# Optimization experiments

Hardware: AMD Instinct MI355X
Metric: run time of the kernel (lower is better)

The kernel has to match this reference:

```python
import jax, jax.numpy as jnp
import numpy as np

B, R = 2, 4096
N_COARSE, N_IMP = 48, 48
RAY_START, RAY_END = 0.1, 1.0
BOX_WARP = 2.0
C_PLANE, H_PLANE = 32, 256
HIDDEN = 64

_P = np.array([[[1, 0, 0], [0, 1, 0], [0, 0, 1]],
               [[1, 0, 0], [0, 0, 1], [0, 1, 0]],
               [[0, 0, 1], [1, 0, 0], [0, 1, 0]]], np.float32)
INV_PLANES = jnp.asarray(np.linalg.inv(_P))  # [3,3,3]


def _gs_one(f, g):
    # f: [C,H,W]; g: [M,2] in [-1,1]; bilinear, zeros padding, align_corners=False
    C, H, W = f.shape
    x = (g[:, 0] + 1.0) * (W / 2) - 0.5
    y = (g[:, 1] + 1.0) * (H / 2) - 0.5
    x0 = jnp.floor(x); y0 = jnp.floor(y)
    xi0 = x0.astype(jnp.int32); yi0 = y0.astype(jnp.int32)
    fx = x - x0; fy = y - y0
    out = jnp.zeros((C, g.shape[0]), f.dtype)
    for dx in (0, 1):
        for dy in (0, 1):
            xi = xi0 + dx; yi = yi0 + dy
            w = (fx if dx else 1.0 - fx) * (fy if dy else 1.0 - fy)
            valid = (xi >= 0) & (xi < W) & (yi >= 0) & (yi < H)
            val = f[:, jnp.clip(yi, 0, H - 1), jnp.clip(xi, 0, W - 1)]  # [C,M]
            out = out + jnp.where(valid, w, 0.0)[None, :] * val
    return out

grid_sample_2d = jax.vmap(_gs_one)


def sample_from_planes(plane_feats, coords):
    # plane_feats [B,3,C,H,W], coords [B,M,3] -> [B,M,C] (mean over planes)
    b, nP, C, H, W = plane_feats.shape
    c = (2.0 / BOX_WARP) * coords
    proj = jnp.einsum('bmk,pkj->bpmj', c, INV_PLANES)[..., :2]  # [B,3,M,2]
    out = grid_sample_2d(plane_feats.reshape(b * nP, C, H, W), proj.reshape(b * nP, -1, 2))
    return out.reshape(b, nP, C, -1).mean(1).transpose(0, 2, 1)


def decoder(tex_f, shp_f, W1, b1, W2, b2):
    x = jnp.concatenate([tex_f, shp_f], -1)          # [B,M,2C]
    h = jax.nn.softplus(x @ W1 + b1)
    o = h @ W2 + b2
    sigma = o[..., :1]
    rgb = jax.nn.sigmoid(o[..., 1:]) * (1 + 2 * 0.001) - 0.001
    return rgb, sigma


def ray_march(colors, densities, depths):
    # MipRayMarcher2: midpoint compositing, softplus(density-1), alpha compositing
    deltas = depths[:, :, 1:] - depths[:, :, :-1]
    c_mid = (colors[:, :, :-1] + colors[:, :, 1:]) * 0.5
    d_mid = (densities[:, :, :-1] + densities[:, :, 1:]) * 0.5
    z_mid = (depths[:, :, :-1] + depths[:, :, 1:]) * 0.5
    dens = jax.nn.softplus(d_mid - 1.0)
    alpha = 1.0 - jnp.exp(-dens * deltas)
    shifted = jnp.concatenate([jnp.ones_like(alpha[:, :, :1]), 1.0 - alpha + 1e-10], 2)
    weights = alpha * jnp.cumprod(shifted, 2)[:, :, :-1]
    rgb = (weights * c_mid).sum(2)
    wt = weights.sum(2)
    depth = jnp.nan_to_num((weights * z_mid).sum(2) / wt, posinf=0.0)
    depth = jnp.clip(depth, depths.min(), depths.max())
    return rgb * 2.0 - 1.0, depth, weights


def sample_pdf(bins, weights, u):
    # bins [P,Nb], weights [P,Nw], u [P,Ni] -> inverse-CDF samples [P,Ni]
    pdf = weights / jnp.sum(weights, -1, keepdims=True)
    cdf = jnp.cumsum(pdf, -1)
    cdf = jnp.concatenate([jnp.zeros_like(cdf[:, :1]), cdf], -1)
    inds = jax.vmap(lambda c, uu: jnp.searchsorted(c, uu, side='right'))(cdf, u)
    below = jnp.maximum(inds - 1, 0)
    above = jnp.minimum(inds, weights.shape[-1])
    cdf0 = jnp.take_along_axis(cdf, below, 1)
    cdf1 = jnp.take_along_axis(cdf, above, 1)
    b0 = jnp.take_along_axis(bins, below, 1)
    b1v = jnp.take_along_axis(bins, above, 1)
    denom = cdf1 - cdf0
    denom = jnp.where(denom < 1e-5, 1.0, denom)
    t = (u - cdf0) / denom
    return b0 + t * (b1v - b0)


def sample_importance(depths, weights, u):
    b, r, n1, _ = weights.shape  # n1 = N_COARSE - 1
    w = weights.reshape(b * r, n1)
    # max_pool1d(k=2, s=1, pad=1) then avg_pool1d(k=2, s=1), then +0.01 (weights >= 0)
    wp = jnp.concatenate([jnp.zeros_like(w[:, :1]), w, jnp.zeros_like(w[:, :1])], 1)
    w = jnp.maximum(wp[:, :-1], wp[:, 1:])
    w = 0.5 * (w[:, :-1] + w[:, 1:]) + 0.01
    z = depths.reshape(b * r, -1)
    z_mid = 0.5 * (z[:, :-1] + z[:, 1:])
    fine = sample_pdf(z_mid, w[:, 1:-1], u.reshape(b * r, -1))
    return jax.lax.stop_gradient(fine.reshape(b, r, -1, 1))  # .detach() in torch


def run_model(planes_tex, planes_shp, coords, W1, b1, W2, b2):
    tex_f = sample_from_planes(planes_tex, coords)
    shp_f = sample_from_planes(planes_shp, coords)
    return decoder(tex_f, shp_f, W1, b1, W2, b2)


def reference(planes_tex, planes_shp, ray_origins, ray_directions, W1, b1, W2, b2, strat_noise, imp_u):
    dirs = ray_directions / jnp.linalg.norm(ray_directions, axis=-1, keepdims=True)
    b, r, _ = ray_origins.shape
    delta = (RAY_END - RAY_START) / (N_COARSE - 1)
    base = RAY_START + delta * jnp.arange(N_COARSE, dtype=jnp.float32)
    depths_c = base.reshape(1, 1, N_COARSE, 1) + strat_noise * delta  # [B,R,Nc,1]
    coords_c = (ray_origins[:, :, None] + depths_c * dirs[:, :, None]).reshape(b, -1, 3)
    rgb_c, sig_c = run_model(planes_tex, planes_shp, coords_c, W1, b1, W2, b2)
    rgb_c = rgb_c.reshape(b, r, N_COARSE, 3)
    sig_c = sig_c.reshape(b, r, N_COARSE, 1)
    _, _, weights = ray_march(rgb_c, sig_c, depths_c)
    depths_f = sample_importance(depths_c, weights, imp_u)  # [B,R,Ni,1]
    coords_f = (ray_origins[:, :, None] + depths_f * dirs[:, :, None]).reshape(b, -1, 3)
    rgb_f, sig_f = run_model(planes_tex, planes_shp, coords_f, W1, b1, W2, b2)
    rgb_f = rgb_f.reshape(b, r, N_IMP, 3)
    sig_f = sig_f.reshape(b, r, N_IMP, 1)
    all_d = jnp.concatenate([depths_c, depths_f], 2)
    all_c = jnp.concatenate([rgb_c, rgb_f], 2)
    all_s = jnp.concatenate([sig_c, sig_f], 2)
    idx = jnp.argsort(all_d, axis=2)
    all_d = jnp.take_along_axis(all_d, idx, 2)
    all_c = jnp.take_along_axis(all_c, jnp.broadcast_to(idx, all_c.shape), 2)
    all_s = jnp.take_along_axis(all_s, idx, 2)
    rgb_final, depth_final, w_all = ray_march(all_c, all_s, all_d)
    return rgb_final, depth_final, w_all.sum(2)


def setup_inputs() -> dict:
    key = jax.random.key(0)
    ks = jax.random.split(key, 8)
    return {
        'planes_tex': jax.random.normal(ks[0], (B, 3, C_PLANE, H_PLANE, H_PLANE), jnp.float32),
        'planes_shp': jax.random.normal(ks[1], (B, 3, C_PLANE, H_PLANE, H_PLANE), jnp.float32),
        'ray_origins': 0.3 * jax.random.normal(ks[2], (B, R, 3), jnp.float32),
        'ray_directions': jax.random.normal(ks[3], (B, R, 3), jnp.float32),
        'W1': jax.random.normal(ks[4], (2 * C_PLANE, HIDDEN), jnp.float32) / np.sqrt(2 * C_PLANE),
        'b1': jnp.zeros((HIDDEN,), jnp.float32),
        'W2': jax.random.normal(ks[5], (HIDDEN, 4), jnp.float32) / np.sqrt(HIDDEN),
        'b2': jnp.zeros((4,), jnp.float32),
        'strat_noise': jax.random.uniform(ks[6], (B, R, N_COARSE, 1), jnp.float32),
        'imp_u': jax.random.uniform(ks[7], (B, R, N_IMP), jnp.float32),
    }
```

## Files before the change

kernel.cpp:

```cpp
#include <hip/hip_runtime.h>
#include <hip/hip_fp16.h>
#include <math.h>

#define NRAY 8192
#define NC_  48
#define NI_  48
#define CPL  32
#define HPL  256
#define HID  64
#define NPTS (NRAY * NC_)

typedef __attribute__((ext_vector_type(8))) short short8;
typedef __attribute__((ext_vector_type(4))) float f32x4;

__device__ __forceinline__ float softplusf(float x) {
    return fmaxf(x, 0.0f) + __logf(1.0f + __expf(-fabsf(x)));
}
__device__ __forceinline__ float sigmoidf(float x) {
    return 1.0f / (1.0f + __expf(-x));
}
__device__ __forceinline__ unsigned short f2bf(float f) {
    unsigned u = __float_as_uint(f);
    u += 0x7fffu + ((u >> 16) & 1u);
    return (unsigned short)(u >> 16);
}

#define TR_BLOCKS 3072
__global__ __launch_bounds__(256) void setup_kernel(
    const float* __restrict__ tex, const float* __restrict__ shp,
    __half* __restrict__ planes_cl,
    const float* __restrict__ W1, const float* __restrict__ b1, const float* __restrict__ W2,
    unsigned short* __restrict__ w1f, float* __restrict__ w2f, float* __restrict__ b1f,
    float* __restrict__ minmax,
    const float* __restrict__ noise, float* __restrict__ depths)
{
    __shared__ __half t2[256][34];
    int b = blockIdx.x;
    int tid = threadIdx.x;
    if (b < TR_BLOCKS) {
        int p = b >> 8;
        int y = b & 255;
        const float* in = (p < 6) ? tex : shp;
        int pp    = (p < 6) ? p : p - 6;
        int choff = (p < 6) ? 0 : 32;
        const float* row = in + ((size_t)(pp * 32) * 256 + y) * 256;
#pragma unroll
        for (int c = 0; c < 32; ++c)
            t2[tid][c] = __float2half(row[(size_t)c * 65536 + tid]);
        __syncthreads();
        __half* outRow = planes_cl + ((size_t)(pp * 256 + y) * 256) * 64 + choff;
#pragma unroll
        for (int it = 0; it < 4; ++it) {
            int idx = it * 256 + tid;
            int x = idx >> 2, c8 = (idx & 3) * 8;
            *(uint4*)(outRow + (size_t)x * 64 + c8) = *(const uint4*)&t2[x][c8];
        }
    } else if (b == TR_BLOCKS) {
        int l = tid;
        if (l == 0) {
            ((int*)minmax)[0] = 0x7f800000;
            ((int*)minmax)[1] = 0xff800000;
        }
        if (l < 64) {
            int g = l >> 4, c = l & 15;
#pragma unroll
            for (int t = 0; t < 4; ++t) {
#pragma unroll
                for (int kb = 0; kb < 2; ++kb)
#pragma unroll
                    for (int j = 0; j < 8; ++j)
                        w1f[((t * 2 + kb) * 64 + l) * 8 + j] =
                            f2bf(W1[(kb * 32 + g * 8 + j) * HID + t * 16 + c]);
#pragma unroll
                for (int o = 0; o < 4; ++o) w2f[(t * 64 + l) * 4 + o] = W2[(t * 16 + c) * 4 + o];
                b1f[t * 64 + l] = b1[t * 16 + c];
            }
        }
    } else {
        int gid = (b - TR_BLOCKS - 1) * 256 + tid;
        if (gid < NPTS) {
            int s = gid % NC_;
            const float delta = (1.0f - 0.1f) / (NC_ - 1);
            depths[gid] = 0.1f + delta * (float)s + noise[gid] * delta;
        }
    }
}

__global__ __launch_bounds__(256, 8) void fused_sample_mlp(
    const __half* __restrict__ planes,
    const float* __restrict__ origins, const float* __restrict__ dirs,
    const float* __restrict__ depths,
    const unsigned short* __restrict__ w1f, const float* __restrict__ w2f,
    const float* __restrict__ b1f, const float* __restrict__ b2,
    float4* __restrict__ outRGBS)
{
    __shared__ unsigned short lds_x[32][72];
    __shared__ int s_tap[32][12][2];

    int tid = threadIdx.x;

    if (tid < 96) {
        int p  = tid & 31;
        int pp = tid >> 5;
        int point = blockIdx.x * 32 + p;
        int ray = point / NC_;
        int bIdx = ray >> 12;

        float ox = origins[ray * 3 + 0], oy = origins[ray * 3 + 1], oz = origins[ray * 3 + 2];
        float dx = dirs[ray * 3 + 0], dy = dirs[ray * 3 + 1], dz = dirs[ray * 3 + 2];
        float invn = 1.0f / sqrtf(dx * dx + dy * dy + dz * dz);
        dx *= invn; dy *= invn; dz *= invn;
        float t = depths[point];
        float px = ox + t * dx, py = oy + t * dy, pz = oz + t * dz;

        float U = (pp == 2) ? pz : px;
        float V = (pp == 0) ? py : ((pp == 1) ? pz : px);
        const float inv3 = 1.0f / 3.0f;

        float gx = (U + 1.0f) * 128.0f - 0.5f;
        float gy = (V + 1.0f) * 128.0f - 0.5f;
        float fgx = floorf(gx), fgy = floorf(gy);
        int x0 = (int)fgx, y0 = (int)fgy;
        float fx = gx - fgx, fy = gy - fgy;
#pragma unroll
        for (int k = 0; k < 4; ++k) {
            int dxk = k & 1, dyk = k >> 1;
            int xi = x0 + dxk, yi = y0 + dyk;
            float w = (dxk ? fx : 1.0f - fx) * (dyk ? fy : 1.0f - fy);
            bool valid = (xi >= 0) && (xi < HPL) && (yi >= 0) && (yi < HPL);
            int xc = min(max(xi, 0), HPL - 1);
            int yc = min(max(yi, 0), HPL - 1);
            int p3 = bIdx * 3 + pp;
            s_tap[p][pp * 4 + k][0] = (((p3 * HPL) + yc) * HPL + xc) * 64;
            s_tap[p][pp * 4 + k][1] = __float_as_int(valid ? w * inv3 : 0.0f);
        }
    }
    __syncthreads();

    {
        int p = tid >> 3, sub = tid & 7;
        int   off[12];
        float wv[12];
#pragma unroll
        for (int kk = 0; kk < 12; ++kk) {
            off[kk] = s_tap[p][kk][0];
            wv[kk]  = __int_as_float(s_tap[p][kk][1]);
        }
        __half2 acc2[4];
#pragma unroll
        for (int i = 0; i < 4; ++i) acc2[i] = __half2half2(__float2half(0.0f));
#pragma unroll
        for (int kk = 0; kk < 12; ++kk) {
            __half2 w2 = __half2half2(__float2half(wv[kk]));
            float4 v = *(const float4*)(planes + off[kk] + sub * 8);
            union { float4 f; __half2 h[4]; } u;
            u.f = v;
#pragma unroll
            for (int i = 0; i < 4; ++i) acc2[i] = __hfma2(u.h[i], w2, acc2[i]);
        }
        unsigned short u16[8];
#pragma unroll
        for (int i = 0; i < 4; ++i) {
            float2 f2 = __half22float2(acc2[i]);
            u16[2 * i]     = f2bf(f2.x);
            u16[2 * i + 1] = f2bf(f2.y);
        }
        *(uint4*)&lds_x[p][sub * 8] = *(uint4*)(u16);
    }
    __syncthreads();

    int lane = tid & 63, wave = tid >> 6;
    if (wave < 2) {
        int g = lane >> 4, c = lane & 15;
        int mrow = wave * 16 + c;
        short8 a0 = *(const short8*)(&lds_x[mrow][g * 8]);
        short8 a1 = *(const short8*)(&lds_x[mrow][32 + g * 8]);

        float o[4][4];
#pragma unroll
        for (int r = 0; r < 4; ++r)
#pragma unroll
            for (int q = 0; q < 4; ++q) o[r][q] = 0.0f;

#pragma unroll
        for (int t = 0; t < 4; ++t) {
            short8 bf0 = *(const short8*)(w1f + ((size_t)((t * 2 + 0) * 64 + lane)) * 8);
            short8 bf1 = *(const short8*)(w1f + ((size_t)((t * 2 + 1) * 64 + lane)) * 8);
            f32x4 z = {0.f, 0.f, 0.f, 0.f};
            z = __builtin_amdgcn_mfma_f32_16x16x32_bf16(a0, bf0, z, 0, 0, 0);
            z = __builtin_amdgcn_mfma_f32_16x16x32_bf16(a1, bf1, z, 0, 0, 0);
            float  b1s = b1f[t * 64 + lane];
            float4 w2  = *(const float4*)(w2f + (size_t)(t * 64 + lane) * 4);
#pragma unroll
            for (int r = 0; r < 4; ++r) {
                float sp = softplusf(z[r] + b1s);
                o[r][0] = fmaf(sp, w2.x, o[r][0]);
                o[r][1] = fmaf(sp, w2.y, o[r][1]);
                o[r][2] = fmaf(sp, w2.z, o[r][2]);
                o[r][3] = fmaf(sp, w2.w, o[r][3]);
            }
        }
#pragma unroll
        for (int mask = 1; mask <= 8; mask <<= 1)
#pragma unroll
            for (int r = 0; r < 4; ++r)
#pragma unroll
                for (int q = 0; q < 4; ++q) o[r][q] += __shfl_xor(o[r][q], mask, 64);

        if (c == 0) {
#pragma unroll
            for (int r = 0; r < 4; ++r) {
                int pt = blockIdx.x * 32 + wave * 16 + g * 4 + r;
                float sig = o[r][0] + b2[0];
                float rr = sigmoidf(o[r][1] + b2[1]) * 1.002f - 0.001f;
                float gg = sigmoidf(o[r][2] + b2[2]) * 1.002f - 0.001f;
                float bb = sigmoidf(o[r][3] + b2[3]) * 1.002f - 0.001f;
                outRGBS[pt] = make_float4(rr, gg, bb, sig);
            }
        }
    }
}

#define CI_WAVES 4
__global__ __launch_bounds__(256) void cdf_imp(
    const float* __restrict__ depths_c, const float4* __restrict__ rgbs_c,
    const float* __restrict__ impu,
    float* __restrict__ depths_f, float* __restrict__ minmax)
{
    __shared__ float s_cdf[CI_WAVES][48];
    __shared__ float s_zm[CI_WAVES][48];
    __shared__ float smn[CI_WAVES], smx[CI_WAVES];
    int wave = threadIdx.x >> 6, lane = threadIdx.x & 63;
    int ray = blockIdx.x * CI_WAVES + wave;

    float d = 0.f, sg = 0.f;
    if (lane < NC_) {
        d  = depths_c[ray * NC_ + lane];
        sg = rgbs_c[ray * NC_ + lane].w;
    }
    float dn = __shfl_down(d, 1, 64);
    float sn = __shfl_down(sg, 1, 64);
    bool iv = (lane < NC_ - 1);

    float zm = 0.5f * (d + dn);
    float alpha = 0.f, f = 1.0f;
    if (iv) {
        float dens = softplusf(0.5f * (sg + sn) - 1.0f);
        alpha = 1.0f - __expf(-dens * (dn - d));
        f = 1.0f - alpha + 1e-10f;
    }
    float x = f;
#pragma unroll
    for (int s = 1; s < 64; s <<= 1) {
        float t = __shfl_up(x, s, 64);
        if (lane >= s) x *= t;
    }
    float excl = __shfl_up(x, 1, 64);
    if (lane == 0) excl = 1.0f;
    float w = alpha * excl;

    float wprev = __shfl_up(w, 1, 64);
    float wmax;
    if (lane == 0) wmax = w;
    else if (lane == NC_ - 1) wmax = wprev;
    else wmax = fmaxf(wprev, w);
    float wmaxn = __shfl_down(wmax, 1, 64);
    float wb = 0.5f * (wmax + wmaxn) + 0.01f;

    float v = (lane >= 1 && lane <= 45) ? wb : 0.0f;
    float s = v;
#pragma unroll
    for (int mask = 1; mask <= 32; mask <<= 1) s += __shfl_xor(s, mask, 64);
    float pdf = v / s;
    float cum = pdf;
#pragma unroll
    for (int st = 1; st < 64; st <<= 1) {
        float t = __shfl_up(cum, st, 64);
        if (lane >= st) cum += t;
    }
    if (lane <= 45) s_cdf[wave][lane] = (lane == 0) ? 0.0f : cum;
    if (iv) s_zm[wave][lane] = zm;

    float d47 = __shfl(d, NC_ - 1, 64);
    if (lane == 0) { smn[wave] = d; smx[wave] = d47; }
    __syncthreads();
    if (threadIdx.x == 0) {
        float mn = smn[0], mx = smx[0];
#pragma unroll
        for (int i = 1; i < CI_WAVES; ++i) { mn = fminf(mn, smn[i]); mx = fmaxf(mx, smx[i]); }
        atomicMin((int*)minmax, __float_as_int(mn));
        atomicMax(((int*)minmax) + 1, __float_as_int(mx));
    }

    if (lane < NI_) {
        const float* cdf = s_cdf[wave];
        const float* zmp = s_zm[wave];
        float u = impu[ray * NI_ + lane];
        int lo = 0, hi = 46;
        while (lo < hi) { int mid = (lo + hi) >> 1; if (cdf[mid] > u) hi = mid; else lo = mid + 1; }
        int below = max(lo - 1, 0);
        int above = min(lo, 45);
        float c0 = cdf[below], c1 = cdf[above];
        float b0 = zmp[below], b1v = zmp[above];
        float den = c1 - c0; if (den < 1e-5f) den = 1.0f;
        depths_f[ray * NI_ + lane] = b0 + (u - c0) / den * (b1v - b0);
    }
}

#define FM_WAVES 4
__global__ __launch_bounds__(256) void final_march(
    const float* __restrict__ depths_c, const float4* __restrict__ rgbs_c,
    const float* __restrict__ depths_f, const float4* __restrict__ rgbs_f,
    const float* __restrict__ minmax, float* __restrict__ out)
{
    __shared__ float s_dc[FM_WAVES][NC_];
    __shared__ float s_df[FM_WAVES][NI_];
    __shared__ float s_md[FM_WAVES][96];
    __shared__ float s_ms[FM_WAVES][96];
    __shared__ float s_mr[FM_WAVES][96];
    __shared__ float s_mg[FM_WAVES][96];
    __shared__ float s_mb[FM_WAVES][96];

    int wave = threadIdx.x >> 6, lane = threadIdx.x & 63;
    int ray = blockIdx.x * FM_WAVES + wave;
    float* dcp = s_dc[wave];
    float* dfp = s_df[wave];
    float* mdp = s_md[wave];
    float* msp = s_ms[wave];
    float* mrp = s_mr[wave];
    float* mgp = s_mg[wave];
    float* mbp = s_mb[wave];

    float dcv = 0.f, dfv = 0.f;
    float4 c4 = make_float4(0, 0, 0, 0), f4 = make_float4(0, 0, 0, 0);
    if (lane < NC_) {
        dcv = depths_c[ray * NC_ + lane];
        dfv = depths_f[ray * NI_ + lane];
        dcp[lane] = dcv;
        dfp[lane] = dfv;
        c4 = rgbs_c[ray * NC_ + lane];
        f4 = rgbs_f[ray * NI_ + lane];
    }
    __syncthreads();

    if (lane < NC_) {
        int cntC = 0, rankF = 0, cntCle = 0;
#pragma unroll
        for (int j = 0; j < NC_; ++j) {
            float dfj = dfp[j];
            float dcj = dcp[j];
            cntC   += (dfj < dcv) ? 1 : 0;
            rankF  += ((dfj < dfv) || (dfj == dfv && j < lane)) ? 1 : 0;
            cntCle += (dcj <= dfv) ? 1 : 0;
        }
        int posC = lane + cntC;
        int posF = rankF + cntCle;
        mdp[posC] = dcv; msp[posC] = c4.w; mrp[posC] = c4.x; mgp[posC] = c4.y; mbp[posC] = c4.z;
        mdp[posF] = dfv; msp[posF] = f4.w; mrp[posF] = f4.x; mgp[posF] = f4.y; mbp[posF] = f4.z;
    }
    __syncthreads();

    int k0 = 2 * lane;
    int i0 = min(k0, 95), i1 = min(k0 + 1, 95), i2 = min(k0 + 2, 95);
    float d0 = mdp[i0], d1 = mdp[i1], d2 = mdp[i2];
    float sg0 = msp[i0], sg1 = msp[i1], sg2 = msp[i2];
    float r0 = mrp[i0], r1 = mrp[i1], r2 = mrp[i2];
    float g0 = mgp[i0], g1 = mgp[i1], g2 = mgp[i2];
    float bb0 = mbp[i0], bb1 = mbp[i1], bb2 = mbp[i2];

    bool v0 = (k0 < 95), v1 = (k0 + 1 < 95);
    float a0 = 0.f, a1 = 0.f, f0 = 1.f, f1 = 1.f;
    if (v0) {
        float dens = softplusf(0.5f * (sg0 + sg1) - 1.0f);
        a0 = 1.0f - __expf(-dens * (d1 - d0));
        f0 = 1.0f - a0 + 1e-10f;
    }
    if (v1) {
        float dens = softplusf(0.5f * (sg1 + sg2) - 1.0f);
        a1 = 1.0f - __expf(-dens * (d2 - d1));
        f1 = 1.0f - a1 + 1e-10f;
    }

    float pl = f0 * f1;
    float x = pl;
#pragma unroll
    for (int d = 1; d < 64; d <<= 1) {
        float t = __shfl_up(x, d, 64);
        if (lane >= d) x *= t;
    }
    float excl = __shfl_up(x, 1, 64);
    if (lane == 0) excl = 1.0f;
    float w0 = a0 * excl;
    float w1 = a1 * excl * f0;

    float accR = w0 * 0.5f * (r0 + r1) + w1 * 0.5f * (r1 + r2);
    float accG = w0 * 0.5f * (g0 + g1) + w1 * 0.5f * (g1 + g2);
    float accB = w0 * 0.5f * (bb0 + bb1) + w1 * 0.5f * (bb1 + bb2);
    float accD = w0 * 0.5f * (d0 + d1) + w1 * 0.5f * (d1 + d2);
    float accW = w0 + w1;
#pragma unroll
    for (int mask = 1; mask <= 32; mask <<= 1) {
        accR += __shfl_xor(accR, mask, 64);
        accG += __shfl_xor(accG, mask, 64);
        accB += __shfl_xor(accB, mask, 64);
        accD += __shfl_xor(accD, mask, 64);
        accW += __shfl_xor(accW, mask, 64);
    }

    if (lane == 0) {
        float q = accD / accW;
        if (!isfinite(q)) q = 0.0f;
        q = fminf(fmaxf(q, minmax[0]), minmax[1]);
        out[ray * 3 + 0] = accR * 2.0f - 1.0f;
        out[ray * 3 + 1] = accG * 2.0f - 1.0f;
        out[ray * 3 + 2] = accB * 2.0f - 1.0f;
        out[3 * NRAY + ray] = q;
        out[4 * NRAY + ray] = accW;
    }
}

extern "C" void kernel_launch(void* const* d_in, const int* in_sizes, int n_in,
                              void* d_out, int out_size, void* d_ws, size_t ws_size,
                              hipStream_t stream)
{
    const float* planes_tex = (const float*)d_in[0];
    const float* planes_shp = (const float*)d_in[1];
    const float* origins    = (const float*)d_in[2];
    const float* raydirs    = (const float*)d_in[3];
    const float* W1 = (const float*)d_in[4];
    const float* b1 = (const float*)d_in[5];
    const float* W2 = (const float*)d_in[6];
    const float* b2 = (const float*)d_in[7];
    const float* noise = (const float*)d_in[8];
    const float* impu  = (const float*)d_in[9];
    float* out = (float*)d_out;

    char* ws = (char*)d_ws;
    __half*         planes_cl = (__half*)ws;
    unsigned short* w1f       = (unsigned short*)(ws + 50331648);
    float*          w2f       = (float*)(ws + 50339840);
    float*          b1f       = (float*)(ws + 50343936);
    float*          minmax    = (float*)(ws + 50345216);
    float*  depths_c = (float*)(ws + 50345472);
    float*  depths_f = depths_c + NPTS;
    float4* rgbs_c   = (float4*)(depths_f + NPTS);
    float4* rgbs_f   = rgbs_c + NPTS;

    int fill_blocks = (NPTS + 255) / 256;
    setup_kernel<<<dim3(TR_BLOCKS + 1 + fill_blocks), dim3(256), 0, stream>>>(
        planes_tex, planes_shp, planes_cl, W1, b1, W2, w1f, w2f, b1f, minmax, noise, depths_c);

    fused_sample_mlp<<<dim3(NPTS / 32), dim3(256), 0, stream>>>(
        planes_cl, origins, raydirs, depths_c, w1f, w2f, b1f, b2, rgbs_c);

    cdf_imp<<<dim3(NRAY / CI_WAVES), dim3(256), 0, stream>>>(depths_c, rgbs_c, impu, depths_f, minmax);

    fused_sample_mlp<<<dim3(NPTS / 32), dim3(256), 0, stream>>>(
        planes_cl, origins, raydirs, depths_f, w1f, w2f, b1f, b2, rgbs_f);

    final_march<<<dim3(NRAY / FM_WAVES), dim3(256), 0, stream>>>(depths_c, rgbs_c, depths_f, rgbs_f, minmax, out);
}
```

Before: 321.2 us.

## Fuse depth generation and importance sampling into the sample-MLP kernels

Coarse depths are now computed inline in the first sample-MLP pass, and the CDF/importance sampling step is folded into the second pass, which builds per-ray CDFs in shared memory before sampling. This removes the separate cdf_imp launch and the depth-fill pass in setup. The global depth min/max atomics are replaced by 16 partial min/max values computed from noise in setup and reduced in final_march. The cost is that each fine block recomputes the CDF for up to two rays, so the same CDF work is redone across blocks, and the block now needs an extra barrier.

```diff
diff --git a/kernel.cpp b/kernel.cpp
--- a/kernel.cpp
+++ b/kernel.cpp
@@ -5,7 +5,6 @@
 #define NRAY 8192
 #define NC_  48
 #define NI_  48
-#define CPL  32
 #define HPL  256
 #define HID  64
 #define NPTS (NRAY * NC_)
@@ -31,10 +30,11 @@
     __half* __restrict__ planes_cl,
     const float* __restrict__ W1, const float* __restrict__ b1, const float* __restrict__ W2,
     unsigned short* __restrict__ w1f, float* __restrict__ w2f, float* __restrict__ b1f,
-    float* __restrict__ minmax,
-    const float* __restrict__ noise, float* __restrict__ depths)
+    float* __restrict__ part_mn, float* __restrict__ part_mx,
+    const float* __restrict__ noise)
 {
     __shared__ __half t2[256][34];
+    __shared__ float smn[4], smx[4];
     int b = blockIdx.x;
     int tid = threadIdx.x;
     if (b < TR_BLOCKS) {
@@ -57,10 +57,6 @@
         }
     } else if (b == TR_BLOCKS) {
         int l = tid;
-        if (l == 0) {
-            ((int*)minmax)[0] = 0x7f800000;
-            ((int*)minmax)[1] = 0xff800000;
-        }
         if (l < 64) {
             int g = l >> 4, c = l & 15;
 #pragma unroll
@@ -77,27 +73,104 @@
             }
         }
     } else {
-        int gid = (b - TR_BLOCKS - 1) * 256 + tid;
-        if (gid < NPTS) {
-            int s = gid % NC_;
+        int bl = b - TR_BLOCKS - 1;
+        int gtid = bl * 256 + tid;
+        float mn = INFINITY, mx = -INFINITY;
+        for (int r = gtid; r < NRAY; r += 4096) {
+            mn = fminf(mn, noise[r * NC_]);
+            mx = fmaxf(mx, noise[r * NC_ + NC_ - 1]);
+        }
+#pragma unroll
+        for (int mask = 1; mask <= 32; mask <<= 1) {
+            mn = fminf(mn, __shfl_xor(mn, mask, 64));
+            mx = fmaxf(mx, __shfl_xor(mx, mask, 64));
+        }
+        int wv = tid >> 6;
+        if ((tid & 63) == 0) { smn[wv] = mn; smx[wv] = mx; }
+        __syncthreads();
+        if (tid == 0) {
+#pragma unroll
+            for (int i = 1; i < 4; ++i) { mn = fminf(mn, smn[i]); mx = fmaxf(mx, smx[i]); }
             const float delta = (1.0f - 0.1f) / (NC_ - 1);
-            depths[gid] = 0.1f + delta * (float)s + noise[gid] * delta;
-        }
-    }
-}
-
+            part_mn[bl] = 0.1f + mn * delta;
+            part_mx[bl] = 0.1f + delta * 47.0f + mx * delta;
+        }
+    }
+}
+
+template<bool FINE>
 __global__ __launch_bounds__(256, 8) void fused_sample_mlp(
     const __half* __restrict__ planes,
     const float* __restrict__ origins, const float* __restrict__ dirs,
-    const float* __restrict__ depths,
+    const float* __restrict__ noise,
+    const float* __restrict__ impu,
+    const float* __restrict__ depths_c,
+    const float4* __restrict__ rgbs_c_in,
+    float* __restrict__ depths_out,
     const unsigned short* __restrict__ w1f, const float* __restrict__ w2f,
     const float* __restrict__ b1f, const float* __restrict__ b2,
     float4* __restrict__ outRGBS)
 {
     __shared__ unsigned short lds_x[32][72];
     __shared__ int s_tap[32][12][2];
+    __shared__ float s_cdf[2][48];
+    __shared__ float s_zm[2][48];
 
     int tid = threadIdx.x;
+    int r0 = (blockIdx.x * 32) / NC_;
+
+    if constexpr (FINE) {
+        int wv = tid >> 6, lane = tid & 63;
+        int r1 = (blockIdx.x * 32 + 31) / NC_;
+        if (wv <= r1 - r0) {
+            int ray = r0 + wv;
+            float d = 0.f, sg = 0.f;
+            if (lane < NC_) {
+                d  = depths_c[ray * NC_ + lane];
+                sg = rgbs_c_in[ray * NC_ + lane].w;
+            }
+            float dn = __shfl_down(d, 1, 64);
+            float sn = __shfl_down(sg, 1, 64);
+            bool iv = (lane < NC_ - 1);
+            float zm = 0.5f * (d + dn);
+            float alpha = 0.f, f = 1.0f;
+            if (iv) {
+                float dens = softplusf(0.5f * (sg + sn) - 1.0f);
+                alpha = 1.0f - __expf(-dens * (dn - d));
+                f = 1.0f - alpha + 1e-10f;
+            }
+            float x = f;
+#pragma unroll
+            for (int s = 1; s < 64; s <<= 1) {
+                float t = __shfl_up(x, s, 64);
+                if (lane >= s) x *= t;
+            }
+            float excl = __shfl_up(x, 1, 64);
+            if (lane == 0) excl = 1.0f;
+            float w = alpha * excl;
+            float wprev = __shfl_up(w, 1, 64);
+            float wmax;
+            if (lane == 0) wmax = w;
+            else if (lane == NC_ - 1) wmax = wprev;
+            else wmax = fmaxf(wprev, w);
+            float wmaxn = __shfl_down(wmax, 1, 64);
+            float wb = 0.5f * (wmax + wmaxn) + 0.01f;
+            float v = (lane >= 1 && lane <= 45) ? wb : 0.0f;
+            float ssum = v;
+#pragma unroll
+            for (int mask = 1; mask <= 32; mask <<= 1) ssum += __shfl_xor(ssum, mask, 64);
+            float pdf = v / ssum;
+            float cum = pdf;
+#pragma unroll
+            for (int st = 1; st < 64; st <<= 1) {
+                float t = __shfl_up(cum, st, 64);
+                if (lane >= st) cum += t;
+            }
+            if (lane <= 45) s_cdf[wv][lane] = (lane == 0) ? 0.0f : cum;
+            if (iv) s_zm[wv][lane] = zm;
+        }
+        __syncthreads();
+    }
 
     if (tid < 96) {
         int p  = tid & 31;
@@ -106,11 +179,31 @@
         int ray = point / NC_;
         int bIdx = ray >> 12;
 
+        float t;
+        if constexpr (!FINE) {
+            int s = point - ray * NC_;
+            const float delta = (1.0f - 0.1f) / (NC_ - 1);
+            t = 0.1f + delta * (float)s + noise[point] * delta;
+        } else {
+            int ridx = ray - r0;
+            float u = impu[point];
+            const float* cdf = s_cdf[ridx];
+            const float* zmp = s_zm[ridx];
+            int lo = 0, hi = 46;
+            while (lo < hi) { int mid = (lo + hi) >> 1; if (cdf[mid] > u) hi = mid; else lo = mid + 1; }
+            int below = max(lo - 1, 0);
+            int above = min(lo, 45);
+            float c0 = cdf[below], c1 = cdf[above];
+            float b0 = zmp[below], b1v = zmp[above];
+            float den = c1 - c0; if (den < 1e-5f) den = 1.0f;
+            t = b0 + (u - c0) / den * (b1v - b0);
+        }
+        if (pp == 0) depths_out[point] = t;
+
         float ox = origins[ray * 3 + 0], oy = origins[ray * 3 + 1], oz = origins[ray * 3 + 2];
         float dx = dirs[ray * 3 + 0], dy = dirs[ray * 3 + 1], dz = dirs[ray * 3 + 2];
         float invn = 1.0f / sqrtf(dx * dx + dy * dy + dz * dz);
         dx *= invn; dy *= invn; dz *= invn;
-        float t = depths[point];
         float px = ox + t * dx, py = oy + t * dy, pz = oz + t * dz;
 
         float U = (pp == 2) ? pz : px;
@@ -221,97 +314,12 @@
     }
 }
 
-#define CI_WAVES 4
-__global__ __launch_bounds__(256) void cdf_imp(
-    const float* __restrict__ depths_c, const float4* __restrict__ rgbs_c,
-    const float* __restrict__ impu,
-    float* __restrict__ depths_f, float* __restrict__ minmax)
-{
-    __shared__ float s_cdf[CI_WAVES][48];
-    __shared__ float s_zm[CI_WAVES][48];
-    __shared__ float smn[CI_WAVES], smx[CI_WAVES];
-    int wave = threadIdx.x >> 6, lane = threadIdx.x & 63;
-    int ray = blockIdx.x * CI_WAVES + wave;
-
-    float d = 0.f, sg = 0.f;
-    if (lane < NC_) {
-        d  = depths_c[ray * NC_ + lane];
-        sg = rgbs_c[ray * NC_ + lane].w;
-    }
-    float dn = __shfl_down(d, 1, 64);
-    float sn = __shfl_down(sg, 1, 64);
-    bool iv = (lane < NC_ - 1);
-
-    float zm = 0.5f * (d + dn);
-    float alpha = 0.f, f = 1.0f;
-    if (iv) {
-        float dens = softplusf(0.5f * (sg + sn) - 1.0f);
-        alpha = 1.0f - __expf(-dens * (dn - d));
-        f = 1.0f - alpha + 1e-10f;
-    }
-    float x = f;
-#pragma unroll
-    for (int s = 1; s < 64; s <<= 1) {
-        float t = __shfl_up(x, s, 64);
-        if (lane >= s) x *= t;
-    }
-    float excl = __shfl_up(x, 1, 64);
-    if (lane == 0) excl = 1.0f;
-    float w = alpha * excl;
-
-    float wprev = __shfl_up(w, 1, 64);
-    float wmax;
-    if (lane == 0) wmax = w;
-    else if (lane == NC_ - 1) wmax = wprev;
-    else wmax = fmaxf(wprev, w);
-    float wmaxn = __shfl_down(wmax, 1, 64);
-    float wb = 0.5f * (wmax + wmaxn) + 0.01f;
-
-    float v = (lane >= 1 && lane <= 45) ? wb : 0.0f;
-    float s = v;
-#pragma unroll
-    for (int mask = 1; mask <= 32; mask <<= 1) s += __shfl_xor(s, mask, 64);
-    float pdf = v / s;
-    float cum = pdf;
-#pragma unroll
-    for (int st = 1; st < 64; st <<= 1) {
-        float t = __shfl_up(cum, st, 64);
-        if (lane >= st) cum += t;
-    }
-    if (lane <= 45) s_cdf[wave][lane] = (lane == 0) ? 0.0f : cum;
-    if (iv) s_zm[wave][lane] = zm;
-
-    float d47 = __shfl(d, NC_ - 1, 64);
-    if (lane == 0) { smn[wave] = d; smx[wave] = d47; }
-    __syncthreads();
-    if (threadIdx.x == 0) {
-        float mn = smn[0], mx = smx[0];
-#pragma unroll
-        for (int i = 1; i < CI_WAVES; ++i) { mn = fminf(mn, smn[i]); mx = fmaxf(mx, smx[i]); }
-        atomicMin((int*)minmax, __float_as_int(mn));
-        atomicMax(((int*)minmax) + 1, __float_as_int(mx));
-    }
-
-    if (lane < NI_) {
-        const float* cdf = s_cdf[wave];
-        const float* zmp = s_zm[wave];
-        float u = impu[ray * NI_ + lane];
-        int lo = 0, hi = 46;
-        while (lo < hi) { int mid = (lo + hi) >> 1; if (cdf[mid] > u) hi = mid; else lo = mid + 1; }
-        int below = max(lo - 1, 0);
-        int above = min(lo, 45);
-        float c0 = cdf[below], c1 = cdf[above];
-        float b0 = zmp[below], b1v = zmp[above];
-        float den = c1 - c0; if (den < 1e-5f) den = 1.0f;
-        depths_f[ray * NI_ + lane] = b0 + (u - c0) / den * (b1v - b0);
-    }
-}
-
 #define FM_WAVES 4
 __global__ __launch_bounds__(256) void final_march(
     const float* __restrict__ depths_c, const float4* __restrict__ rgbs_c,
     const float* __restrict__ depths_f, const float4* __restrict__ rgbs_f,
-    const float* __restrict__ minmax, float* __restrict__ out)
+    const float* __restrict__ part_mn, const float* __restrict__ part_mx,
+    float* __restrict__ out)
 {
     __shared__ float s_dc[FM_WAVES][NC_];
     __shared__ float s_df[FM_WAVES][NI_];
@@ -407,10 +415,18 @@
         accW += __shfl_xor(accW, mask, 64);
     }
 
+    float pmn = (lane < 16) ? part_mn[lane] : INFINITY;
+    float pmx = (lane < 16) ? part_mx[lane] : -INFINITY;
+#pragma unroll
+    for (int mask = 1; mask <= 32; mask <<= 1) {
+        pmn = fminf(pmn, __shfl_xor(pmn, mask, 64));
+        pmx = fmaxf(pmx, __shfl_xor(pmx, mask, 64));
+    }
+
     if (lane == 0) {
         float q = accD / accW;
         if (!isfinite(q)) q = 0.0f;
-        q = fminf(fmaxf(q, minmax[0]), minmax[1]);
+        q = fminf(fmaxf(q, pmn), pmx);
         out[ray * 3 + 0] = accR * 2.0f - 1.0f;
         out[ray * 3 + 1] = accG * 2.0f - 1.0f;
         out[ray * 3 + 2] = accB * 2.0f - 1.0f;
@@ -440,23 +456,24 @@
     unsigned short* w1f       = (unsigned short*)(ws + 50331648);
     float*          w2f       = (float*)(ws + 50339840);
     float*          b1f       = (float*)(ws + 50343936);
-    float*          minmax    = (float*)(ws + 50345216);
-    float*  depths_c = (float*)(ws + 50345472);
-    float*  depths_f = depths_c + NPTS;
-    float4* rgbs_c   = (float4*)(depths_f + NPTS);
-    float4* rgbs_f   = rgbs_c + NPTS;
-
-    int fill_blocks = (NPTS + 255) / 256;
-    setup_kernel<<<dim3(TR_BLOCKS + 1 + fill_blocks), dim3(256), 0, stream>>>(
-        planes_tex, planes_shp, planes_cl, W1, b1, W2, w1f, w2f, b1f, minmax, noise, depths_c);
-
-    fused_sample_mlp<<<dim3(NPTS / 32), dim3(256), 0, stream>>>(
-        planes_cl, origins, raydirs, depths_c, w1f, w2f, b1f, b2, rgbs_c);
-
-    cdf_imp<<<dim3(NRAY / CI_WAVES), dim3(256), 0, stream>>>(depths_c, rgbs_c, impu, depths_f, minmax);
-
-    fused_sample_mlp<<<dim3(NPTS / 32), dim3(256), 0, stream>>>(
-        planes_cl, origins, raydirs, depths_f, w1f, w2f, b1f, b2, rgbs_f);
-
-    final_march<<<dim3(NRAY / FM_WAVES), dim3(256), 0, stream>>>(depths_c, rgbs_c, depths_f, rgbs_f, minmax, out);
-}
+    float*          part_mn   = (float*)(ws + 50344960);
+    float*          part_mx   = (float*)(ws + 50345024);
+    float*  depths_c = (float*)(ws + 50345216);
+    float*  depths_f = (float*)(ws + 51918080);
+    float4* rgbs_c   = (float4*)(ws + 53490944);
+    float4* rgbs_f   = (float4*)(ws + 59782400);
+
+    setup_kernel<<<dim3(TR_BLOCKS + 1 + 16), dim3(256), 0, stream>>>(
+        planes_tex, planes_shp, planes_cl, W1, b1, W2, w1f, w2f, b1f, part_mn, part_mx, noise);
+
+    fused_sample_mlp<false><<<dim3(NPTS / 32), dim3(256), 0, stream>>>(
+        planes_cl, origins, raydirs, noise, nullptr, nullptr, nullptr,
+        depths_c, w1f, w2f, b1f, b2, rgbs_c);
+
+    fused_sample_mlp<true><<<dim3(NPTS / 32), dim3(256), 0, stream>>>(
+        planes_cl, origins, raydirs, nullptr, impu, depths_c, rgbs_c,
+        depths_f, w1f, w2f, b1f, b2, rgbs_f);
+
+    final_march<<<dim3(NRAY / FM_WAVES), dim3(256), 0, stream>>>(
+        depths_c, rgbs_c, depths_f, rgbs_f, part_mn, part_mx, out);
+}
```

Result: faster. 282.7 us (-12.0%).
